# Kernel tuning notes

Hardware: AMD Instinct MI355X
Metric: run time of the kernel (lower is better)

Reference implementation:

```python
import jax, jax.numpy as jnp
import numpy as np

B = 16384
C = 2048  # in_channel
OUT = 2   # out_channel


def setup_inputs() -> dict:
    key = jax.random.key(0)
    k1, k2, k3, k4, k5, k6, k7 = jax.random.split(key, 7)
    scale = 1.0 / np.sqrt(3 * C)  # torch Linear default init range
    return {
        "s_f": jax.random.normal(k1, (B, C), dtype=jnp.float32),
        "g_f": jax.random.normal(k2, (B, C), dtype=jnp.float32),
        "v_f": jax.random.normal(k3, (B, C), dtype=jnp.float32),
        "W_aff": jax.random.uniform(k4, (3 * C, 3), dtype=jnp.float32, minval=-scale, maxval=scale),
        "b_aff": jax.random.uniform(k5, (3,), dtype=jnp.float32, minval=-scale, maxval=scale),
        "W_cls": jax.random.uniform(k6, (3 * C, OUT), dtype=jnp.float32, minval=-scale, maxval=scale),
        "b_cls": jax.random.uniform(k7, (OUT,), dtype=jnp.float32, minval=-scale, maxval=scale),
    }


def reference(s_f, g_f, v_f, W_aff, b_aff, W_cls, b_cls):
    # Attention gating over the three modalities.
    x_att = jnp.concatenate([s_f, g_f, v_f], axis=1)          # [B, 3C]
    att = jax.nn.softmax(x_att @ W_aff + b_aff, axis=1)       # [B, 3]
    # diag(att[:, i]) @ f  ==  per-row scalar scaling (broadcast multiply).
    s = att[:, 0:1] * s_f
    g = att[:, 1:2] * g_f
    v = att[:, 2:3] * v_f
    x = jnp.concatenate([s, g, v], axis=1)                    # [B, 3C]
    return jax.nn.softmax(x @ W_cls + b_cls, axis=1)          # [B, OUT]
```

## Files before the change

### kernel.cpp

```cpp
#include <hip/hip_runtime.h>

#define B_ROWS 16384
#define C_DIM  2048
#define BLK    512
#define CHUNK  4
#define RPB    16
#define GROUP  8
#define NWAVE  (BLK / 64)

#define DPP_ADD(v, ctrl, rmask) \
  v += __int_as_float(__builtin_amdgcn_update_dpp(0, __float_as_int(v), (ctrl), (rmask), 0xf, false))

__device__ __forceinline__ float wave_sum64(float v) {
  DPP_ADD(v, 0x111, 0xf);
  DPP_ADD(v, 0x112, 0xf);
  DPP_ADD(v, 0x114, 0xf);
  DPP_ADD(v, 0x118, 0xf);
  DPP_ADD(v, 0x142, 0xa);
  DPP_ADD(v, 0x143, 0xc);
  return v;
}

__global__ __launch_bounds__(BLK, 4)
void maff_fused(const float* __restrict__ s_f,
                const float* __restrict__ g_f,
                const float* __restrict__ v_f,
                const float* __restrict__ W_aff,
                const float* __restrict__ b_aff,
                const float* __restrict__ W_cls,
                const float* __restrict__ b_cls,
                float* __restrict__ out)
{
  const int t    = threadIdx.x;
  const int lane = t & 63;
  const int wave = t >> 6;
  const int c0   = t * CHUNK;

  float waf[3][12];
  float wcf[3][8];
#pragma unroll
  for (int m = 0; m < 3; ++m) {
    const float4* pa = (const float4*)(W_aff + (size_t)(m * C_DIM + c0) * 3);
    float4 a0 = pa[0], a1 = pa[1], a2 = pa[2];
    waf[m][0]=a0.x; waf[m][1]=a0.y; waf[m][2]=a0.z; waf[m][3]=a0.w;
    waf[m][4]=a1.x; waf[m][5]=a1.y; waf[m][6]=a1.z; waf[m][7]=a1.w;
    waf[m][8]=a2.x; waf[m][9]=a2.y; waf[m][10]=a2.z; waf[m][11]=a2.w;
    const float4* pc = (const float4*)(W_cls + (size_t)(m * C_DIM + c0) * 2);
    float4 q0 = pc[0], q1 = pc[1];
    wcf[m][0]=q0.x; wcf[m][1]=q0.y; wcf[m][2]=q0.z; wcf[m][3]=q0.w;
    wcf[m][4]=q1.x; wcf[m][5]=q1.y; wcf[m][6]=q1.z; wcf[m][7]=q1.w;
  }
  const float ba0 = b_aff[0], ba1 = b_aff[1], ba2 = b_aff[2];
  const float bc0 = b_cls[0], bc1 = b_cls[1];

  __shared__ float red[2][GROUP][NWAVE][9];

  const int row0 = blockIdx.x * RPB;

  float4 cs, cg, cv;
  {
    const size_t off = (size_t)row0 * C_DIM + c0;
    cs = *(const float4*)(s_f + off);
    cg = *(const float4*)(g_f + off);
    cv = *(const float4*)(v_f + off);
  }

  for (int r = 0; r < RPB; ++r) {
    const int    pr   = row0 + ((r + 1 < RPB) ? (r + 1) : r);
    const size_t poff = (size_t)pr * C_DIM + c0;
    float4 ns = *(const float4*)(s_f + poff);
    float4 ng = *(const float4*)(g_f + poff);
    float4 nv = *(const float4*)(v_f + poff);

    float fs[CHUNK] = {cs.x, cs.y, cs.z, cs.w};
    float fg[CHUNK] = {cg.x, cg.y, cg.z, cg.w};
    float fv[CHUNK] = {cv.x, cv.y, cv.z, cv.w};

    float a0=0.f, a1=0.f, a2=0.f;
    float d00=0.f, d01=0.f, d10=0.f, d11=0.f, d20=0.f, d21=0.f;
#pragma unroll
    for (int i = 0; i < CHUNK; ++i) {
      a0  = fmaf(fs[i], waf[0][i*3+0], a0);
      a1  = fmaf(fs[i], waf[0][i*3+1], a1);
      a2  = fmaf(fs[i], waf[0][i*3+2], a2);
      a0  = fmaf(fg[i], waf[1][i*3+0], a0);
      a1  = fmaf(fg[i], waf[1][i*3+1], a1);
      a2  = fmaf(fg[i], waf[1][i*3+2], a2);
      a0  = fmaf(fv[i], waf[2][i*3+0], a0);
      a1  = fmaf(fv[i], waf[2][i*3+1], a1);
      a2  = fmaf(fv[i], waf[2][i*3+2], a2);
      d00 = fmaf(fs[i], wcf[0][i*2+0], d00);
      d01 = fmaf(fs[i], wcf[0][i*2+1], d01);
      d10 = fmaf(fg[i], wcf[1][i*2+0], d10);
      d11 = fmaf(fg[i], wcf[1][i*2+1], d11);
      d20 = fmaf(fv[i], wcf[2][i*2+0], d20);
      d21 = fmaf(fv[i], wcf[2][i*2+1], d21);
    }

    a0  = wave_sum64(a0);  a1  = wave_sum64(a1);  a2  = wave_sum64(a2);
    d00 = wave_sum64(d00); d01 = wave_sum64(d01);
    d10 = wave_sum64(d10); d11 = wave_sum64(d11);
    d20 = wave_sum64(d20); d21 = wave_sum64(d21);

    const int gslot = r & (GROUP - 1);
    const int gbuf  = (r >> 3) & 1;
    if (lane == 63) {
      float* dst = &red[gbuf][gslot][wave][0];
      dst[0] = a0;  dst[1] = a1;  dst[2] = a2;
      dst[3] = d00; dst[4] = d01; dst[5] = d10;
      dst[6] = d11; dst[7] = d20; dst[8] = d21;
    }

    if (gslot == GROUP - 1) {
      __syncthreads();
      if (t < GROUP) {
        const float* q = &red[gbuf][t][0][0];
        float A0=ba0, A1=ba1, A2=ba2;
        float D00=0.f, D01=0.f, D10=0.f, D11=0.f, D20=0.f, D21=0.f;
#pragma unroll
        for (int w = 0; w < NWAVE; ++w) {
          const float* p = q + w * 9;
          A0 += p[0]; A1 += p[1]; A2 += p[2];
          D00 += p[3]; D01 += p[4]; D10 += p[5];
          D11 += p[6]; D20 += p[7]; D21 += p[8];
        }

        float mx = fmaxf(A0, fmaxf(A1, A2));
        float e0 = __expf(A0 - mx), e1 = __expf(A1 - mx), e2 = __expf(A2 - mx);
        float inv = 1.0f / (e0 + e1 + e2);
        float t0 = e0 * inv, t1 = e1 * inv, t2 = e2 * inv;

        float L0 = t0 * D00 + t1 * D10 + t2 * D20 + bc0;
        float L1 = t0 * D01 + t1 * D11 + t2 * D21 + bc1;
        float mm = fmaxf(L0, L1);
        float x0 = __expf(L0 - mm), x1 = __expf(L1 - mm);
        float is = 1.0f / (x0 + x1);

        const int row = row0 + (r - (GROUP - 1)) + t;
        *(float2*)(out + (size_t)row * 2) = make_float2(x0 * is, x1 * is);
      }
    }

    cs = ns; cg = ng; cv = nv;
  }
}

extern "C" void kernel_launch(void* const* d_in, const int* in_sizes, int n_in,
                              void* d_out, int out_size, void* d_ws, size_t ws_size,
                              hipStream_t stream) {
  const float* s_f   = (const float*)d_in[0];
  const float* g_f   = (const float*)d_in[1];
  const float* v_f   = (const float*)d_in[2];
  const float* W_aff = (const float*)d_in[3];
  const float* b_aff = (const float*)d_in[4];
  const float* W_cls = (const float*)d_in[5];
  const float* b_cls = (const float*)d_in[6];
  float* out = (float*)d_out;

  dim3 grid(B_ROWS / RPB);
  dim3 block(BLK);
  maff_fused<<<grid, block, 0, stream>>>(s_f, g_f, v_f, W_aff, b_aff, W_cls, b_cls, out);
}
```

Measured before the change: 378.5 us.

## Split fused kernel into per-modality partial-dot kernel plus epilogue

The single fused kernel is split in two. The first kernel gives each of the three modalities its own grid dimension, so each block streams one input tensor with 8 contiguous floats per thread and accumulates 5 partial dot products per row. Partial sums go to a workspace buffer, and a small second kernel combines them and computes both softmaxes. This cuts per-thread register use and the number of concurrent load streams, aiming for higher occupancy and simpler access patterns. The cost is an extra kernel launch and a workspace round trip.

Result: faster. 366.3 us (-3.2%).

```diff
diff --git a/kernel.cpp b/kernel.cpp
--- a/kernel.cpp
+++ b/kernel.cpp
@@ -2,11 +2,11 @@
 
 #define B_ROWS 16384
 #define C_DIM  2048
-#define BLK    512
-#define CHUNK  4
-#define RPB    16
+#define BLK    256
+#define CPT    8
+#define RPB    32
 #define GROUP  8
-#define NWAVE  (BLK / 64)
+#define NACC   5
 
 #define DPP_ADD(v, ctrl, rmask) \
   v += __int_as_float(__builtin_amdgcn_update_dpp(0, __float_as_int(v), (ctrl), (rmask), 0xf, false))
@@ -21,128 +21,131 @@
   return v;
 }
 
-__global__ __launch_bounds__(BLK, 4)
-void maff_fused(const float* __restrict__ s_f,
-                const float* __restrict__ g_f,
-                const float* __restrict__ v_f,
-                const float* __restrict__ W_aff,
-                const float* __restrict__ b_aff,
-                const float* __restrict__ W_cls,
-                const float* __restrict__ b_cls,
-                float* __restrict__ out)
+__global__ __launch_bounds__(BLK, 6)
+void maff_partial(const float* __restrict__ s_f,
+                  const float* __restrict__ g_f,
+                  const float* __restrict__ v_f,
+                  const float* __restrict__ W_aff,
+                  const float* __restrict__ W_cls,
+                  float* __restrict__ ws)
 {
   const int t    = threadIdx.x;
   const int lane = t & 63;
   const int wave = t >> 6;
-  const int c0   = t * CHUNK;
+  const int m    = blockIdx.y;
+  const int row0 = blockIdx.x * RPB;
+  const int c0   = t * CPT;
 
-  float waf[3][12];
-  float wcf[3][8];
-#pragma unroll
-  for (int m = 0; m < 3; ++m) {
-    const float4* pa = (const float4*)(W_aff + (size_t)(m * C_DIM + c0) * 3);
-    float4 a0 = pa[0], a1 = pa[1], a2 = pa[2];
-    waf[m][0]=a0.x; waf[m][1]=a0.y; waf[m][2]=a0.z; waf[m][3]=a0.w;
-    waf[m][4]=a1.x; waf[m][5]=a1.y; waf[m][6]=a1.z; waf[m][7]=a1.w;
-    waf[m][8]=a2.x; waf[m][9]=a2.y; waf[m][10]=a2.z; waf[m][11]=a2.w;
-    const float4* pc = (const float4*)(W_cls + (size_t)(m * C_DIM + c0) * 2);
-    float4 q0 = pc[0], q1 = pc[1];
-    wcf[m][0]=q0.x; wcf[m][1]=q0.y; wcf[m][2]=q0.z; wcf[m][3]=q0.w;
-    wcf[m][4]=q1.x; wcf[m][5]=q1.y; wcf[m][6]=q1.z; wcf[m][7]=q1.w;
-  }
-  const float ba0 = b_aff[0], ba1 = b_aff[1], ba2 = b_aff[2];
-  const float bc0 = b_cls[0], bc1 = b_cls[1];
+  const float* f = (m == 0) ? s_f : (m == 1) ? g_f : v_f;
 
-  __shared__ float red[2][GROUP][NWAVE][9];
-
-  const int row0 = blockIdx.x * RPB;
-
-  float4 cs, cg, cv;
+  float wa[CPT][3];
+  float wc[CPT][2];
   {
-    const size_t off = (size_t)row0 * C_DIM + c0;
-    cs = *(const float4*)(s_f + off);
-    cg = *(const float4*)(g_f + off);
-    cv = *(const float4*)(v_f + off);
+    const float4* pa = (const float4*)(W_aff + ((size_t)m * C_DIM + c0) * 3);
+    float4 a0 = pa[0], a1 = pa[1], a2 = pa[2], a3 = pa[3], a4 = pa[4], a5 = pa[5];
+    wa[0][0]=a0.x; wa[0][1]=a0.y; wa[0][2]=a0.z;
+    wa[1][0]=a0.w; wa[1][1]=a1.x; wa[1][2]=a1.y;
+    wa[2][0]=a1.z; wa[2][1]=a1.w; wa[2][2]=a2.x;
+    wa[3][0]=a2.y; wa[3][1]=a2.z; wa[3][2]=a2.w;
+    wa[4][0]=a3.x; wa[4][1]=a3.y; wa[4][2]=a3.z;
+    wa[5][0]=a3.w; wa[5][1]=a4.x; wa[5][2]=a4.y;
+    wa[6][0]=a4.z; wa[6][1]=a4.w; wa[6][2]=a5.x;
+    wa[7][0]=a5.y; wa[7][1]=a5.z; wa[7][2]=a5.w;
+    const float4* pc = (const float4*)(W_cls + ((size_t)m * C_DIM + c0) * 2);
+    float4 q0 = pc[0], q1 = pc[1], q2 = pc[2], q3 = pc[3];
+    wc[0][0]=q0.x; wc[0][1]=q0.y; wc[1][0]=q0.z; wc[1][1]=q0.w;
+    wc[2][0]=q1.x; wc[2][1]=q1.y; wc[3][0]=q1.z; wc[3][1]=q1.w;
+    wc[4][0]=q2.x; wc[4][1]=q2.y; wc[5][0]=q2.z; wc[5][1]=q2.w;
+    wc[6][0]=q3.x; wc[6][1]=q3.y; wc[7][0]=q3.z; wc[7][1]=q3.w;
   }
 
+  __shared__ float red[2][GROUP][4][NACC];
+
+  const float* b0 = f + (size_t)row0 * C_DIM + c0;
+  float4 cx0 = ((const float4*)b0)[0];
+  float4 cx1 = ((const float4*)b0)[1];
+
   for (int r = 0; r < RPB; ++r) {
-    const int    pr   = row0 + ((r + 1 < RPB) ? (r + 1) : r);
-    const size_t poff = (size_t)pr * C_DIM + c0;
-    float4 ns = *(const float4*)(s_f + poff);
-    float4 ng = *(const float4*)(g_f + poff);
-    float4 nv = *(const float4*)(v_f + poff);
+    const int    nr = (r + 1 < RPB) ? (r + 1) : r;
+    const float* nb = f + (size_t)(row0 + nr) * C_DIM + c0;
+    float4 nx0 = ((const float4*)nb)[0];
+    float4 nx1 = ((const float4*)nb)[1];
 
-    float fs[CHUNK] = {cs.x, cs.y, cs.z, cs.w};
-    float fg[CHUNK] = {cg.x, cg.y, cg.z, cg.w};
-    float fv[CHUNK] = {cv.x, cv.y, cv.z, cv.w};
+    float x[CPT] = {cx0.x, cx0.y, cx0.z, cx0.w, cx1.x, cx1.y, cx1.z, cx1.w};
 
-    float a0=0.f, a1=0.f, a2=0.f;
-    float d00=0.f, d01=0.f, d10=0.f, d11=0.f, d20=0.f, d21=0.f;
+    float p0 = 0.f, p1 = 0.f, p2 = 0.f, q0 = 0.f, q1 = 0.f;
 #pragma unroll
-    for (int i = 0; i < CHUNK; ++i) {
-      a0  = fmaf(fs[i], waf[0][i*3+0], a0);
-      a1  = fmaf(fs[i], waf[0][i*3+1], a1);
-      a2  = fmaf(fs[i], waf[0][i*3+2], a2);
-      a0  = fmaf(fg[i], waf[1][i*3+0], a0);
-      a1  = fmaf(fg[i], waf[1][i*3+1], a1);
-      a2  = fmaf(fg[i], waf[1][i*3+2], a2);
-      a0  = fmaf(fv[i], waf[2][i*3+0], a0);
-      a1  = fmaf(fv[i], waf[2][i*3+1], a1);
-      a2  = fmaf(fv[i], waf[2][i*3+2], a2);
-      d00 = fmaf(fs[i], wcf[0][i*2+0], d00);
-      d01 = fmaf(fs[i], wcf[0][i*2+1], d01);
-      d10 = fmaf(fg[i], wcf[1][i*2+0], d10);
-      d11 = fmaf(fg[i], wcf[1][i*2+1], d11);
-      d20 = fmaf(fv[i], wcf[2][i*2+0], d20);
-      d21 = fmaf(fv[i], wcf[2][i*2+1], d21);
+    for (int i = 0; i < CPT; ++i) {
+      p0 = fmaf(x[i], wa[i][0], p0);
+      p1 = fmaf(x[i], wa[i][1], p1);
+      p2 = fmaf(x[i], wa[i][2], p2);
+      q0 = fmaf(x[i], wc[i][0], q0);
+      q1 = fmaf(x[i], wc[i][1], q1);
     }
 
-    a0  = wave_sum64(a0);  a1  = wave_sum64(a1);  a2  = wave_sum64(a2);
-    d00 = wave_sum64(d00); d01 = wave_sum64(d01);
-    d10 = wave_sum64(d10); d11 = wave_sum64(d11);
-    d20 = wave_sum64(d20); d21 = wave_sum64(d21);
+    p0 = wave_sum64(p0); p1 = wave_sum64(p1); p2 = wave_sum64(p2);
+    q0 = wave_sum64(q0); q1 = wave_sum64(q1);
 
-    const int gslot = r & (GROUP - 1);
-    const int gbuf  = (r >> 3) & 1;
+    const int gs = r & (GROUP - 1);
+    const int gb = (r >> 3) & 1;
     if (lane == 63) {
-      float* dst = &red[gbuf][gslot][wave][0];
-      dst[0] = a0;  dst[1] = a1;  dst[2] = a2;
-      dst[3] = d00; dst[4] = d01; dst[5] = d10;
-      dst[6] = d11; dst[7] = d20; dst[8] = d21;
+      float* d = &red[gb][gs][wave][0];
+      d[0] = p0; d[1] = p1; d[2] = p2; d[3] = q0; d[4] = q1;
     }
 
-    if (gslot == GROUP - 1) {
+    if (gs == GROUP - 1) {
       __syncthreads();
       if (t < GROUP) {
-        const float* q = &red[gbuf][t][0][0];
-        float A0=ba0, A1=ba1, A2=ba2;
-        float D00=0.f, D01=0.f, D10=0.f, D11=0.f, D20=0.f, D21=0.f;
-#pragma unroll
-        for (int w = 0; w < NWAVE; ++w) {
-          const float* p = q + w * 9;
-          A0 += p[0]; A1 += p[1]; A2 += p[2];
-          D00 += p[3]; D01 += p[4]; D10 += p[5];
-          D11 += p[6]; D20 += p[7]; D21 += p[8];
-        }
-
-        float mx = fmaxf(A0, fmaxf(A1, A2));
-        float e0 = __expf(A0 - mx), e1 = __expf(A1 - mx), e2 = __expf(A2 - mx);
-        float inv = 1.0f / (e0 + e1 + e2);
-        float t0 = e0 * inv, t1 = e1 * inv, t2 = e2 * inv;
-
-        float L0 = t0 * D00 + t1 * D10 + t2 * D20 + bc0;
-        float L1 = t0 * D01 + t1 * D11 + t2 * D21 + bc1;
-        float mm = fmaxf(L0, L1);
-        float x0 = __expf(L0 - mm), x1 = __expf(L1 - mm);
-        float is = 1.0f / (x0 + x1);
-
+        const float* z = &red[gb][t][0][0];
+        float s0 = z[0] + z[5] + z[10] + z[15];
+        float s1 = z[1] + z[6] + z[11] + z[16];
+        float s2 = z[2] + z[7] + z[12] + z[17];
+        float s3 = z[3] + z[8] + z[13] + z[18];
+        float s4 = z[4] + z[9] + z[14] + z[19];
         const int row = row0 + (r - (GROUP - 1)) + t;
-        *(float2*)(out + (size_t)row * 2) = make_float2(x0 * is, x1 * is);
+        ws[(m * 5 + 0) * B_ROWS + row] = s0;
+        ws[(m * 5 + 1) * B_ROWS + row] = s1;
+        ws[(m * 5 + 2) * B_ROWS + row] = s2;
+        ws[(m * 5 + 3) * B_ROWS + row] = s3;
+        ws[(m * 5 + 4) * B_ROWS + row] = s4;
       }
     }
 
-    cs = ns; cg = ng; cv = nv;
+    cx0 = nx0; cx1 = nx1;
   }
+}
+
+__global__ __launch_bounds__(BLK)
+void maff_epilogue(const float* __restrict__ ws,
+                   const float* __restrict__ b_aff,
+                   const float* __restrict__ b_cls,
+                   float* __restrict__ out)
+{
+  const int row = blockIdx.x * BLK + threadIdx.x;
+
+  float P[3][NACC];
+#pragma unroll
+  for (int m = 0; m < 3; ++m)
+#pragma unroll
+    for (int j = 0; j < NACC; ++j)
+      P[m][j] = ws[(m * NACC + j) * B_ROWS + row];
+
+  float A0 = P[0][0] + P[1][0] + P[2][0] + b_aff[0];
+  float A1 = P[0][1] + P[1][1] + P[2][1] + b_aff[1];
+  float A2 = P[0][2] + P[1][2] + P[2][2] + b_aff[2];
+
+  float mx = fmaxf(A0, fmaxf(A1, A2));
+  float e0 = __expf(A0 - mx), e1 = __expf(A1 - mx), e2 = __expf(A2 - mx);
+  float inv = 1.0f / (e0 + e1 + e2);
+  float t0 = e0 * inv, t1 = e1 * inv, t2 = e2 * inv;
+
+  float L0 = t0 * P[0][3] + t1 * P[1][3] + t2 * P[2][3] + b_cls[0];
+  float L1 = t0 * P[0][4] + t1 * P[1][4] + t2 * P[2][4] + b_cls[1];
+  float mm = fmaxf(L0, L1);
+  float x0 = __expf(L0 - mm), x1 = __expf(L1 - mm);
+  float is = 1.0f / (x0 + x1);
+
+  *(float2*)(out + (size_t)row * 2) = make_float2(x0 * is, x1 * is);
 }
 
 extern "C" void kernel_launch(void* const* d_in, const int* in_sizes, int n_in,
@@ -156,8 +159,11 @@
   const float* W_cls = (const float*)d_in[5];
   const float* b_cls = (const float*)d_in[6];
   float* out = (float*)d_out;
+  float* ws  = (float*)d_ws;
 
-  dim3 grid(B_ROWS / RPB);
-  dim3 block(BLK);
-  maff_fused<<<grid, block, 0, stream>>>(s_f, g_f, v_f, W_aff, b_aff, W_cls, b_cls, out);
+  dim3 grid1(B_ROWS / RPB, 3);
+  maff_partial<<<grid1, dim3(BLK), 0, stream>>>(s_f, g_f, v_f, W_aff, W_cls, ws);
+
+  dim3 grid2(B_ROWS / BLK);
+  maff_epilogue<<<grid2, dim3(BLK), 0, stream>>>(ws, b_aff, b_cls, out);
 }
```
